# Optimization experiments

Measured on AMD Instinct MI355X. Metric: run time of the kernel, lower is better.

## Reference

```python
import jax, jax.numpy as jnp
import numpy as np

OBS, H, Z = 64, 128, 64
T, B = 512, 1024
EPS = 0.01


def _lin(x, W, b):
    # torch nn.Linear: y = x @ W.T + b, W: [out, in]
    return x @ W.T + b


def setup_inputs() -> dict:
    key = jax.random.key(0)
    ks = jax.random.split(key, 16)
    n = lambda k, shape: 0.1 * jax.random.normal(k, shape, dtype=jnp.float32)
    z = lambda shape: jnp.zeros(shape, dtype=jnp.float32)
    return {
        "s": jax.random.normal(ks[0], (T, B, OBS), dtype=jnp.float32),
        "noise": jax.random.normal(ks[1], (T, B, Z), dtype=jnp.float32),
        # phi_s / phi_z
        "W_phi_s": n(ks[2], (H, OBS)), "b_phi_s": z((H,)),
        "W_phi_z": n(ks[3], (H, Z)), "b_phi_z": z((H,)),
        # prior: Linear(H,H) ReLU Linear(H,2Z)
        "Wp1": n(ks[4], (H, H)), "bp1": z((H,)),
        "Wp2": n(ks[5], (2 * Z, H)), "bp2": z((2 * Z,)),
        # encoder: Linear(2H,H) ReLU Linear(H,2Z)
        "We1": n(ks[6], (H, 2 * H)), "be1": z((H,)),
        "We2": n(ks[7], (2 * Z, H)), "be2": z((2 * Z,)),
        # LSTMCell(input=2H, hidden=H), gate order i,f,g,o
        "W_ih": n(ks[8], (4 * H, 2 * H)), "b_ih": z((4 * H,)),
        "W_hh": n(ks[9], (4 * H, H)), "b_hh": z((4 * H,)),
        # decoder: Linear(2H,H) ReLU Linear(H,OBS)
        "Wd1": n(ks[10], (H, 2 * H)), "bd1": z((H,)),
        "Wd2": n(ks[11], (OBS, H)), "bd2": z((OBS,)),
    }


def reference(s, noise, W_phi_s, b_phi_s, W_phi_z, b_phi_z, Wp1, bp1, Wp2, bp2,
              We1, be1, We2, be2, W_ih, b_ih, W_hh, b_hh, Wd1, bd1, Wd2, bd2):
    h0 = jnp.zeros((s.shape[1], H), dtype=s.dtype)
    c0 = jnp.zeros((s.shape[1], H), dtype=s.dtype)

    def step(carry, xs):
        h, c, kl_acc, rc_acc = carry
        s_t, n_t = xs
        phi_s = _lin(s_t, W_phi_s, b_phi_s)                      # [B, H]
        # encoder on [phi_s, h]
        enc = _lin(jax.nn.relu(_lin(jnp.concatenate([phi_s, h], -1), We1, be1)), We2, be2)
        z_mu, z_std = jnp.split(enc, 2, axis=-1)
        z_std = jax.nn.softplus(z_std)
        # prior on h
        pri = _lin(jax.nn.relu(_lin(h, Wp1, bp1)), Wp2, bp2)
        p_mu, p_std = jnp.split(pri, 2, axis=-1)
        p_std = jax.nn.softplus(p_std)
        # reparameterize
        z_samp = z_mu + z_std * n_t
        phi_z = _lin(z_samp, W_phi_z, b_phi_z)                   # [B, H]
        # decode from [phi_z, h]
        recon = _lin(jax.nn.relu(_lin(jnp.concatenate([phi_z, h], -1), Wd1, bd1)), Wd2, bd2)
        # LSTM cell update with input [phi_s, phi_z]
        gates = _lin(jnp.concatenate([phi_s, phi_z], -1), W_ih, b_ih) + _lin(h, W_hh, b_hh)
        gi, gf, gg, go = jnp.split(gates, 4, axis=-1)
        c_new = jax.nn.sigmoid(gf) * c + jax.nn.sigmoid(gi) * jnp.tanh(gg)
        h_new = jax.nn.sigmoid(go) * jnp.tanh(c_new)
        # losses (sum over feature dim, mean over batch)
        rc_t = (0.5 * jnp.square(recon - s_t)).sum(-1).mean()
        kl_t = 0.5 * (2.0 * jnp.log(p_std + EPS) - 2.0 * jnp.log(z_std + EPS)
                      + (jnp.square(z_std) + jnp.square(z_mu - p_mu))
                      / (jnp.square(jnp.exp(p_std)) - 1.0)).sum(-1).mean()
        return (h_new, c_new, kl_acc + kl_t, rc_acc + rc_t), None

    (_, _, total_kl, total_rc), _ = jax.lax.scan(
        step, (h0, c0, jnp.float32(0.0), jnp.float32(0.0)), (s, noise))
    return total_kl + total_rc
```

## Files before the change

### kernel.cpp

```cpp
#include <hip/hip_runtime.h>

typedef __bf16 bf16_t;
typedef bf16_t bf16x8 __attribute__((ext_vector_type(8)));
typedef float  f32x4  __attribute__((ext_vector_type(4)));

#define TT 512
#define BB 1024

#define cL0   0
#define cL1   1024
#define cL2   3072
#define cL3   5120
#define cL4   7168
#define cL5   9216
#define cL6   10240
#define cL7   12288
#define cL8   13312
#define cL9   17408
#define cL10  21504
#define NCHUNK 29696

#define WS_FBIAS_OFF 475136
#define WS_FOLD_OFF  478208
#define WS_HSEQ_OFF  1048576
#define WS_NEED (WS_HSEQ_OFF + (size_t)TT * BB * 128 * 2)

__device__ __forceinline__ f32x4 mfma16(bf16x8 a, bf16x8 b, f32x4 c) {
  return __builtin_amdgcn_mfma_f32_16x16x32_bf16(a, b, c, 0, 0, 0);
}
__device__ __forceinline__ float sigm(float x) { return 1.0f / (1.0f + __expf(-x)); }
__device__ __forceinline__ float tanh_f(float x) {
  x = fminf(fmaxf(x, -15.0f), 15.0f);
  float e = __expf(2.0f * x);
  return (e - 1.0f) / (e + 1.0f);
}
__device__ __forceinline__ float softplus_f(float x) {
  return (x > 15.0f) ? x : __logf(1.0f + __expf(x));
}
__device__ __forceinline__ void wg_barrier() {
  asm volatile("s_waitcnt lgkmcnt(0)\n\ts_barrier" ::: "memory");
}
__device__ __forceinline__ void keep(bf16x8& v) { asm volatile("" : "+v"(v)); }

__global__ void vrnn_fold(const float* __restrict__ We1, const float* __restrict__ Wd1,
                          const float* __restrict__ Wih,
                          const float* __restrict__ Wps, const float* __restrict__ Wpz,
                          const float* __restrict__ bps, const float* __restrict__ bpz,
                          const float* __restrict__ be1, const float* __restrict__ bd1,
                          const float* __restrict__ bih, const float* __restrict__ bhh,
                          float* __restrict__ fold, float* __restrict__ fbias) {
  int id = blockIdx.x * 256 + threadIdx.x;
  if (id < 8192) {
    int n = id >> 6, k = id & 63; float acc = 0.f;
    for (int j = 0; j < 128; ++j) acc += We1[n*256 + j] * Wps[j*64 + k];
    fold[id] = acc;
  } else if (id < 16384) {
    int q = id - 8192; int n = q >> 6, k = q & 63; float acc = 0.f;
    for (int j = 0; j < 128; ++j) acc += Wd1[n*256 + j] * Wpz[j*64 + k];
    fold[id] = acc;
  } else if (id < 49152) {
    int q = id - 16384; int n = q >> 6, k = q & 63; float acc = 0.f;
    for (int j = 0; j < 128; ++j) acc += Wih[n*256 + j] * Wps[j*64 + k];
    fold[id] = acc;
  } else if (id < 81920) {
    int q = id - 49152; int n = q >> 6, k = q & 63; float acc = 0.f;
    for (int j = 0; j < 128; ++j) acc += Wih[n*256 + 128 + j] * Wpz[j*64 + k];
    fold[id] = acc;
  } else if (id < 82048) {
    int n = id - 81920; float acc = be1[n];
    for (int j = 0; j < 128; ++j) acc += We1[n*256 + j] * bps[j];
    fbias[n] = acc;
  } else if (id < 82176) {
    int n = id - 82048; float acc = bd1[n];
    for (int j = 0; j < 128; ++j) acc += Wd1[n*256 + j] * bpz[j];
    fbias[128 + n] = acc;
  } else if (id < 82688) {
    int n = id - 82176; float acc = bih[n] + bhh[n];
    for (int j = 0; j < 128; ++j) acc += Wih[n*256 + j]*bps[j] + Wih[n*256 + 128 + j]*bpz[j];
    fbias[256 + n] = acc;
  }
}

__global__ void vrnn_pack(const float* __restrict__ fold,
                          const float* __restrict__ We1, const float* __restrict__ We2,
                          const float* __restrict__ Wp1, const float* __restrict__ Wp2,
                          const float* __restrict__ Wd1, const float* __restrict__ Wd2,
                          const float* __restrict__ Whh,
                          bf16_t* __restrict__ packed) {
  int c = blockIdx.x * 256 + threadIdx.x;
  if (c >= NCHUNK) return;
  const float* src; int rs, co, Kt, base;
  if      (c < 1024)  { base = cL0;  src = fold;          rs = 64;  co = 0;   Kt = 2; }
  else if (c < 3072)  { base = cL1;  src = We1;           rs = 256; co = 128; Kt = 4; }
  else if (c < 5120)  { base = cL2;  src = We2;           rs = 128; co = 0;   Kt = 4; }
  else if (c < 7168)  { base = cL3;  src = Wp1;           rs = 128; co = 0;   Kt = 4; }
  else if (c < 9216)  { base = cL4;  src = Wp2;           rs = 128; co = 0;   Kt = 4; }
  else if (c < 10240) { base = cL5;  src = fold + 8192;   rs = 64;  co = 0;   Kt = 2; }
  else if (c < 12288) { base = cL6;  src = Wd1;           rs = 256; co = 128; Kt = 4; }
  else if (c < 13312) { base = cL7;  src = Wd2;           rs = 128; co = 0;   Kt = 4; }
  else if (c < 17408) { base = cL8;  src = fold + 16384;  rs = 64;  co = 0;   Kt = 2; }
  else if (c < 21504) { base = cL9;  src = fold + 49152;  rs = 64;  co = 0;   Kt = 2; }
  else                { base = cL10; src = Whh;           rs = 128; co = 0;   Kt = 4; }
  int local = c - base;
  int nt = local / (Kt * 64);
  int r = local - nt * Kt * 64;
  int kt = r >> 6, lane = r & 63;
  int n = nt * 16 + (lane & 15);
  int k = kt * 32 + (lane >> 4) * 8;
  const float* p = src + n * rs + co + k;
  bf16x8 v;
  #pragma unroll
  for (int j = 0; j < 8; ++j) v[j] = (bf16_t)p[j];
  *(bf16x8*)(packed + (size_t)c * 8) = v;
}

__global__ __launch_bounds__(512, 2) void vrnn_loop(
    const float* __restrict__ s, const float* __restrict__ noise,
    const bf16_t* __restrict__ packed, const float* __restrict__ fbias,
    const float* __restrict__ be2, bf16_t* __restrict__ hseq) {
  const bf16x8* Wf = (const bf16x8*)packed;

  __shared__ __align__(16) bf16_t A_h[2][16 * 136];
  __shared__ __align__(16) bf16_t A_s[2][16 * 72];
  __shared__ __align__(16) bf16_t A_z[16 * 72];
  __shared__ __align__(16) bf16_t A_e1[16 * 136];
  __shared__ float bsm[768];

  const int tid  = threadIdx.x;
  const int wv   = tid >> 6, ln = tid & 63;
  const int quad = ln >> 4, col = ln & 15;
  const int row0 = blockIdx.x * 16;
  const int pm_  = tid >> 5;
  const int pj   = (tid & 31) * 2;
  const int nloc0 = wv * 16 + col;
  const int j_own = wv * 16 + col;
  const int wq   = wv & 3;

  for (int i = tid; i < 768; i += 512) {
    float v;
    if      (i < 128) v = fbias[i];
    else if (i < 256) v = be2[i - 128];
    else              v = fbias[256 + (i - 256)];
    bsm[i] = v;
  }
  for (int i = tid; i < 16 * 136; i += 512) A_h[0][i] = (bf16_t)0.0f;
  {
    float2 v = *(const float2*)(s + ((size_t)0 * BB + row0 + pm_) * 64 + pj);
    A_s[0][pm_ * 72 + pj]     = (bf16_t)v.x;
    A_s[0][pm_ * 72 + pj + 1] = (bf16_t)v.y;
  }
  {
    unsigned long long* p = (unsigned long long*)(hseq + (size_t)row0 * 128);
    p[tid] = 0ull;
  }

  bf16x8 rb10[4][4];
  #pragma unroll
  for (int i = 0; i < 4; ++i) {
    int nt = wv + 8 * i;
    #pragma unroll
    for (int k = 0; k < 4; ++k) { rb10[i][k] = Wf[cL10 + (nt * 4 + k) * 64 + ln]; keep(rb10[i][k]); }
  }
  bf16x8 wE[6], rb8[4][2];
  wE[0] = Wf[cL0 + (wv * 2 + 0) * 64 + ln];
  wE[1] = Wf[cL0 + (wv * 2 + 1) * 64 + ln];
  #pragma unroll
  for (int k = 0; k < 4; ++k) wE[2 + k] = Wf[cL1 + (wv * 4 + k) * 64 + ln];
  #pragma unroll
  for (int i = 0; i < 4; ++i) {
    int nt = wv + 8 * i;
    rb8[i][0] = Wf[cL8 + (nt * 2 + 0) * 64 + ln];
    rb8[i][1] = Wf[cL8 + (nt * 2 + 1) * 64 + ln];
  }

  f32x4 c_reg = {0.f, 0.f, 0.f, 0.f};
  __syncthreads();

  int cb = 0;
  for (int t = 0; t < TT; ++t) {
    const int sb = t & 1;
    int zo = 0;
    asm volatile("" : "+s"(zo));
    const bf16x8* Wfv = Wf + zo;

    bf16x8 wmu[4], wsd[4];
    float nzr[4];
    if (wv < 4) {
      #pragma unroll
      for (int k = 0; k < 4; ++k) {
        wmu[k] = Wfv[cL2 + (wq * 4 + k) * 64 + ln];
        wsd[k] = Wfv[cL2 + ((wq + 4) * 4 + k) * 64 + ln];
      }
      #pragma unroll
      for (int r = 0; r < 4; ++r)
        nzr[r] = noise[((size_t)t * BB + row0 + quad * 4 + r) * 64 + j_own];
    }
    float2 svv = make_float2(0.f, 0.f);
    if (t + 1 < TT) svv = *(const float2*)(s + ((size_t)(t + 1) * BB + row0 + pm_) * 64 + pj);

    bf16x8 ah0 = *(const bf16x8*)&A_h[cb][col * 136 + 0 + quad * 8];
    bf16x8 ah1 = *(const bf16x8*)&A_h[cb][col * 136 + 32 + quad * 8];
    bf16x8 ah2 = *(const bf16x8*)&A_h[cb][col * 136 + 64 + quad * 8];
    bf16x8 ah3 = *(const bf16x8*)&A_h[cb][col * 136 + 96 + quad * 8];
    bf16x8 as0 = *(const bf16x8*)&A_s[sb][col * 72 + 0 + quad * 8];
    bf16x8 as1 = *(const bf16x8*)&A_s[sb][col * 72 + 32 + quad * 8];

    {
      float bv = bsm[nloc0];
      f32x4 c = {bv, bv, bv, bv};
      c = mfma16(as0, wE[0], c);
      c = mfma16(as1, wE[1], c);
      c = mfma16(ah0, wE[2], c);
      c = mfma16(ah1, wE[3], c);
      c = mfma16(ah2, wE[4], c);
      c = mfma16(ah3, wE[5], c);
      #pragma unroll
      for (int r = 0; r < 4; ++r)
        A_e1[(quad * 4 + r) * 136 + nloc0] = (bf16_t)fmaxf(c[r], 0.0f);
    }
    f32x4 Cg[4];
    #pragma unroll
    for (int i = 0; i < 4; ++i) {
      float bv = bsm[256 + j_own + 128 * i];
      f32x4 cc = {bv, bv, bv, bv};
      cc = mfma16(ah0, rb10[i][0], cc);
      cc = mfma16(ah1, rb10[i][1], cc);
      cc = mfma16(ah2, rb10[i][2], cc);
      cc = mfma16(ah3, rb10[i][3], cc);
      cc = mfma16(as0, rb8[i][0], cc);
      cc = mfma16(as1, rb8[i][1], cc);
      Cg[i] = cc;
    }
    wg_barrier();

    bf16x8 rb9[4][2];
    #pragma unroll
    for (int i = 0; i < 4; ++i) {
      int nt = wv + 8 * i;
      rb9[i][0] = Wfv[cL9 + (nt * 2 + 0) * 64 + ln];
      rb9[i][1] = Wfv[cL9 + (nt * 2 + 1) * 64 + ln];
    }
    if (wv < 4) {
      bf16x8 ae0 = *(const bf16x8*)&A_e1[col * 136 + 0 + quad * 8];
      bf16x8 ae1 = *(const bf16x8*)&A_e1[col * 136 + 32 + quad * 8];
      bf16x8 ae2 = *(const bf16x8*)&A_e1[col * 136 + 64 + quad * 8];
      bf16x8 ae3 = *(const bf16x8*)&A_e1[col * 136 + 96 + quad * 8];
      float bm = bsm[128 + wq * 16 + col], bs = bsm[128 + 64 + wq * 16 + col];
      f32x4 cm = {bm, bm, bm, bm};
      f32x4 cs = {bs, bs, bs, bs};
      cm = mfma16(ae0, wmu[0], cm); cs = mfma16(ae0, wsd[0], cs);
      cm = mfma16(ae1, wmu[1], cm); cs = mfma16(ae1, wsd[1], cs);
      cm = mfma16(ae2, wmu[2], cm); cs = mfma16(ae2, wsd[2], cs);
      cm = mfma16(ae3, wmu[3], cm); cs = mfma16(ae3, wsd[3], cs);
      #pragma unroll
      for (int r = 0; r < 4; ++r) {
        float z = cm[r] + softplus_f(cs[r]) * nzr[r];
        A_z[(quad * 4 + r) * 72 + wq * 16 + col] = (bf16_t)z;
      }
    }
    if (t + 1 < TT) {
      A_s[sb ^ 1][pm_ * 72 + pj]     = (bf16_t)svv.x;
      A_s[sb ^ 1][pm_ * 72 + pj + 1] = (bf16_t)svv.y;
    }
    wg_barrier();

    wE[0] = Wfv[cL0 + (wv * 2 + 0) * 64 + ln];
    wE[1] = Wfv[cL0 + (wv * 2 + 1) * 64 + ln];
    #pragma unroll
    for (int k = 0; k < 4; ++k) wE[2 + k] = Wfv[cL1 + (wv * 4 + k) * 64 + ln];
    #pragma unroll
    for (int i = 0; i < 4; ++i) {
      int nt = wv + 8 * i;
      rb8[i][0] = Wfv[cL8 + (nt * 2 + 0) * 64 + ln];
      rb8[i][1] = Wfv[cL8 + (nt * 2 + 1) * 64 + ln];
    }
    {
      bf16x8 az0 = *(const bf16x8*)&A_z[col * 72 + 0 + quad * 8];
      bf16x8 az1 = *(const bf16x8*)&A_z[col * 72 + 32 + quad * 8];
      #pragma unroll
      for (int i = 0; i < 4; ++i) {
        Cg[i] = mfma16(az0, rb9[i][0], Cg[i]);
        Cg[i] = mfma16(az1, rb9[i][1], Cg[i]);
      }
    }
    bf16_t* hp = hseq + (size_t)(t + 1) * BB * 128;
    #pragma unroll
    for (int r = 0; r < 4; ++r) {
      float gi = sigm(Cg[0][r]);
      float gf = sigm(Cg[1][r]);
      float gg = tanh_f(Cg[2][r]);
      float go = sigm(Cg[3][r]);
      float cn = gf * c_reg[r] + gi * gg;
      c_reg[r] = cn;
      bf16_t hv = (bf16_t)(go * tanh_f(cn));
      A_h[cb ^ 1][(quad * 4 + r) * 136 + j_own] = hv;
      if (t + 1 < TT) hp[(size_t)(row0 + quad * 4 + r) * 128 + j_own] = hv;
    }
    wg_barrier();
    cb ^= 1;
  }
}

__global__ __launch_bounds__(512, 2) void vrnn_tail(
    const float* __restrict__ s, const float* __restrict__ noise,
    const bf16_t* __restrict__ packed, const float* __restrict__ fbias,
    const float* __restrict__ bp1, const float* __restrict__ bp2,
    const float* __restrict__ be2, const float* __restrict__ bd2,
    const bf16_t* __restrict__ hseq, float* __restrict__ out) {
  const bf16x8* Wf = (const bf16x8*)packed;

  __shared__ __align__(16) bf16_t A_h[16 * 136];
  __shared__ __align__(16) bf16_t A_s[16 * 72];
  __shared__ __align__(16) bf16_t A_z[16 * 72];
  __shared__ __align__(16) bf16_t A_e1[16 * 136];
  __shared__ __align__(16) bf16_t A_p1[16 * 136];
  __shared__ __align__(16) bf16_t A_d1[16 * 136];
  __shared__ float zmu_s[16 * 68], zsd_s[16 * 68];
  __shared__ float dec2o[16 * 68];
  __shared__ float bsm[704];
  __shared__ float red[8];

  const int tid  = threadIdx.x;
  const int wv   = tid >> 6, ln = tid & 63;
  const int quad = ln >> 4, col = ln & 15;
  const int pm_  = tid >> 5;
  const int pj   = (tid & 31) * 2;
  const int nloc0 = wv * 16 + col;
  const int wq   = wv & 3;

  for (int i = tid; i < 704; i += 512) {
    float v;
    if      (i < 128) v = fbias[i];
    else if (i < 256) v = bp1[i - 128];
    else if (i < 384) v = be2[i - 256];
    else if (i < 512) v = bp2[i - 384];
    else if (i < 640) v = fbias[128 + (i - 512)];
    else              v = bd2[i - 640];
    bsm[i] = v;
  }

  bf16x8 wE[6], wP1[4], wmu[4], wsd[4], wD1[4], w5[2], w7[4];
  wE[0] = Wf[cL0 + (wv * 2 + 0) * 64 + ln];
  wE[1] = Wf[cL0 + (wv * 2 + 1) * 64 + ln];
  #pragma unroll
  for (int k = 0; k < 4; ++k) {
    wE[2 + k] = Wf[cL1 + (wv * 4 + k) * 64 + ln];
    wP1[k] = Wf[cL3 + (wv * 4 + k) * 64 + ln];
    wD1[k] = Wf[cL6 + (wv * 4 + k) * 64 + ln];
    w7[k]  = Wf[cL7 + (wq * 4 + k) * 64 + ln];
  }
  {
    int base2 = (wv < 4) ? cL2 : cL4;
    #pragma unroll
    for (int k = 0; k < 4; ++k) {
      wmu[k] = Wf[base2 + (wq * 4 + k) * 64 + ln];
      wsd[k] = Wf[base2 + ((wq + 4) * 4 + k) * 64 + ln];
    }
  }
  w5[0] = Wf[cL5 + (wv * 2 + 0) * 64 + ln];
  w5[1] = Wf[cL5 + (wv * 2 + 1) * 64 + ln];
  #pragma unroll
  for (int k = 0; k < 6; ++k) keep(wE[k]);
  #pragma unroll
  for (int k = 0; k < 4; ++k) { keep(wP1[k]); keep(wmu[k]); keep(wsd[k]); keep(wD1[k]); keep(w7[k]); }
  keep(w5[0]); keep(w5[1]);

  float kl_acc = 0.0f, rc_acc = 0.0f;
  __syncthreads();

  const int hm  = tid >> 5;
  const int hc4 = (tid & 31) * 4;

  for (int tau = blockIdx.x; tau < TT * 64; tau += gridDim.x) {
    const int t = tau >> 6;
    const int row0 = (tau & 63) * 16;

    {
      unsigned long long hv = *(const unsigned long long*)(
          hseq + (size_t)t * BB * 128 + (size_t)(row0 + hm) * 128 + hc4);
      *(unsigned long long*)&A_h[hm * 136 + hc4] = hv;
    }
    float2 sv = *(const float2*)(s + ((size_t)t * BB + row0 + pm_) * 64 + pj);
    A_s[pm_ * 72 + pj]     = (bf16_t)sv.x;
    A_s[pm_ * 72 + pj + 1] = (bf16_t)sv.y;
    float nzr[4];
    if (wv < 4) {
      #pragma unroll
      for (int r = 0; r < 4; ++r)
        nzr[r] = noise[((size_t)t * BB + row0 + quad * 4 + r) * 64 + wq * 16 + col];
    }
    wg_barrier();

    bf16x8 ah0 = *(const bf16x8*)&A_h[col * 136 + 0 + quad * 8];
    bf16x8 ah1 = *(const bf16x8*)&A_h[col * 136 + 32 + quad * 8];
    bf16x8 ah2 = *(const bf16x8*)&A_h[col * 136 + 64 + quad * 8];
    bf16x8 ah3 = *(const bf16x8*)&A_h[col * 136 + 96 + quad * 8];
    bf16x8 as0 = *(const bf16x8*)&A_s[col * 72 + 0 + quad * 8];
    bf16x8 as1 = *(const bf16x8*)&A_s[col * 72 + 32 + quad * 8];
    {
      float bv = bsm[nloc0];
      f32x4 c = {bv, bv, bv, bv};
      c = mfma16(as0, wE[0], c);
      c = mfma16(as1, wE[1], c);
      c = mfma16(ah0, wE[2], c);
      c = mfma16(ah1, wE[3], c);
      c = mfma16(ah2, wE[4], c);
      c = mfma16(ah3, wE[5], c);
      #pragma unroll
      for (int r = 0; r < 4; ++r)
        A_e1[(quad * 4 + r) * 136 + nloc0] = (bf16_t)fmaxf(c[r], 0.0f);
    }
    {
      float bv = bsm[128 + nloc0];
      f32x4 c = {bv, bv, bv, bv};
      c = mfma16(ah0, wP1[0], c);
      c = mfma16(ah1, wP1[1], c);
      c = mfma16(ah2, wP1[2], c);
      c = mfma16(ah3, wP1[3], c);
      #pragma unroll
      for (int r = 0; r < 4; ++r)
        A_p1[(quad * 4 + r) * 136 + nloc0] = (bf16_t)fmaxf(c[r], 0.0f);
    }
    wg_barrier();

    float Pmu[4], Pps[4];
    if (wv < 4) {
      bf16x8 ae0 = *(const bf16x8*)&A_e1[col * 136 + 0 + quad * 8];
      bf16x8 ae1 = *(const bf16x8*)&A_e1[col * 136 + 32 + quad * 8];
      bf16x8 ae2 = *(const bf16x8*)&A_e1[col * 136 + 64 + quad * 8];
      bf16x8 ae3 = *(const bf16x8*)&A_e1[col * 136 + 96 + quad * 8];
      float bm = bsm[256 + wq * 16 + col], bs = bsm[256 + 64 + wq * 16 + col];
      f32x4 cm = {bm, bm, bm, bm};
      f32x4 cs = {bs, bs, bs, bs};
      cm = mfma16(ae0, wmu[0], cm); cs = mfma16(ae0, wsd[0], cs);
      cm = mfma16(ae1, wmu[1], cm); cs = mfma16(ae1, wsd[1], cs);
      cm = mfma16(ae2, wmu[2], cm); cs = mfma16(ae2, wsd[2], cs);
      cm = mfma16(ae3, wmu[3], cm); cs = mfma16(ae3, wsd[3], cs);
      #pragma unroll
      for (int r = 0; r < 4; ++r) {
        float zm = cm[r];
        float zs = softplus_f(cs[r]);
        int m = quad * 4 + r;
        A_z[m * 72 + wq * 16 + col] = (bf16_t)(zm + zs * nzr[r]);
        zmu_s[m * 68 + wq * 16 + col] = zm;
        zsd_s[m * 68 + wq * 16 + col] = zs;
      }
    } else {
      bf16x8 ap0 = *(const bf16x8*)&A_p1[col * 136 + 0 + quad * 8];
      bf16x8 ap1 = *(const bf16x8*)&A_p1[col * 136 + 32 + quad * 8];
      bf16x8 ap2 = *(const bf16x8*)&A_p1[col * 136 + 64 + quad * 8];
      bf16x8 ap3 = *(const bf16x8*)&A_p1[col * 136 + 96 + quad * 8];
      float bm = bsm[384 + wq * 16 + col], bs = bsm[384 + 64 + wq * 16 + col];
      f32x4 cm = {bm, bm, bm, bm};
      f32x4 cs = {bs, bs, bs, bs};
      cm = mfma16(ap0, wmu[0], cm); cs = mfma16(ap0, wsd[0], cs);
      cm = mfma16(ap1, wmu[1], cm); cs = mfma16(ap1, wsd[1], cs);
      cm = mfma16(ap2, wmu[2], cm); cs = mfma16(ap2, wsd[2], cs);
      cm = mfma16(ap3, wmu[3], cm); cs = mfma16(ap3, wsd[3], cs);
      #pragma unroll
      for (int r = 0; r < 4; ++r) { Pmu[r] = cm[r]; Pps[r] = softplus_f(cs[r]); }
    }
    wg_barrier();

    {
      bf16x8 az0 = *(const bf16x8*)&A_z[col * 72 + 0 + quad * 8];
      bf16x8 az1 = *(const bf16x8*)&A_z[col * 72 + 32 + quad * 8];
      float bv = bsm[512 + nloc0];
      f32x4 c = {bv, bv, bv, bv};
      c = mfma16(az0, w5[0], c);
      c = mfma16(az1, w5[1], c);
      c = mfma16(ah0, wD1[0], c);
      c = mfma16(ah1, wD1[1], c);
      c = mfma16(ah2, wD1[2], c);
      c = mfma16(ah3, wD1[3], c);
      #pragma unroll
      for (int r = 0; r < 4; ++r)
        A_d1[(quad * 4 + r) * 136 + nloc0] = (bf16_t)fmaxf(c[r], 0.0f);
    }
    if (wv >= 4) {
      #pragma unroll
      for (int r = 0; r < 4; ++r) {
        int m = quad * 4 + r;
        float zm = zmu_s[m * 68 + wq * 16 + col];
        float zs = zsd_s[m * 68 + wq * 16 + col];
        float dm = zm - Pmu[r];
        float ps = Pps[r];
        float den = __expf(2.0f * ps) - 1.0f;
        kl_acc += 0.5f * (2.0f * __logf(ps + 0.01f) - 2.0f * __logf(zs + 0.01f)
                          + (zs * zs + dm * dm) / den);
      }
    }
    wg_barrier();

    if (wv >= 4) {
      bf16x8 ad0 = *(const bf16x8*)&A_d1[col * 136 + 0 + quad * 8];
      bf16x8 ad1 = *(const bf16x8*)&A_d1[col * 136 + 32 + quad * 8];
      bf16x8 ad2 = *(const bf16x8*)&A_d1[col * 136 + 64 + quad * 8];
      bf16x8 ad3 = *(const bf16x8*)&A_d1[col * 136 + 96 + quad * 8];
      float bv = bsm[640 + wq * 16 + col];
      f32x4 c = {bv, bv, bv, bv};
      c = mfma16(ad0, w7[0], c);
      c = mfma16(ad1, w7[1], c);
      c = mfma16(ad2, w7[2], c);
      c = mfma16(ad3, w7[3], c);
      #pragma unroll
      for (int r = 0; r < 4; ++r)
        dec2o[(quad * 4 + r) * 68 + wq * 16 + col] = c[r];
    }
    wg_barrier();
    {
      float d0 = dec2o[pm_ * 68 + pj] - sv.x;
      float d1 = dec2o[pm_ * 68 + pj + 1] - sv.y;
      rc_acc += 0.5f * (d0 * d0 + d1 * d1);
    }
  }

  float tot = (kl_acc + rc_acc) * (1.0f / 1024.0f);
  #pragma unroll
  for (int off = 32; off > 0; off >>= 1) tot += __shfl_down(tot, off);
  if (ln == 0) red[wv] = tot;
  __syncthreads();
  if (tid == 0) {
    float sum = 0.f;
    #pragma unroll
    for (int i = 0; i < 8; ++i) sum += red[i];
    atomicAdd(out, sum);
  }
}

__global__ __launch_bounds__(512, 2) void vrnn_mono(
    const float* __restrict__ s, const float* __restrict__ noise,
    const bf16_t* __restrict__ packed, const float* __restrict__ fbias,
    const float* __restrict__ bp1, const float* __restrict__ bp2,
    const float* __restrict__ be2, const float* __restrict__ bd2,
    float* __restrict__ out) {
  const bf16x8* Wf = (const bf16x8*)packed;
  __shared__ __align__(16) bf16_t A_h[16 * 136];
  __shared__ __align__(16) bf16_t A_s[2][16 * 72];
  __shared__ __align__(16) bf16_t A_z[16 * 72];
  __shared__ __align__(16) bf16_t A_e1[16 * 136];
  __shared__ __align__(16) bf16_t A_p1[16 * 136];
  __shared__ __align__(16) bf16_t A_d1[16 * 136];
  __shared__ float zmu_s[16 * 68], zsd_s[16 * 68];
  __shared__ float dec2o[16 * 68];
  __shared__ float bsm[1216];
  __shared__ float red[8];
  const int tid  = threadIdx.x;
  const int wv   = tid >> 6, ln = tid & 63;
  const int quad = ln >> 4, col = ln & 15;
  const int row0 = blockIdx.x * 16;
  const int pm_  = tid >> 5;
  const int pj   = (tid & 31) * 2;
  const int nloc0 = wv * 16 + col;
  const int j_own = wv * 16 + col;
  const int wq   = wv & 3;
  for (int i = tid; i < 1216; i += 512) {
    float v;
    if      (i < 128)  v = fbias[i];
    else if (i < 256)  v = bp1[i - 128];
    else if (i < 384)  v = be2[i - 256];
    else if (i < 512)  v = bp2[i - 384];
    else if (i < 640)  v = fbias[128 + (i - 512)];
    else if (i < 704)  v = bd2[i - 640];
    else               v = fbias[256 + (i - 704)];
    bsm[i] = v;
  }
  for (int i = tid; i < 16 * 136; i += 512) A_h[i] = (bf16_t)0.0f;
  {
    float2 v = *(const float2*)(s + ((size_t)0 * BB + row0 + pm_) * 64 + pj);
    A_s[0][pm_ * 72 + pj]     = (bf16_t)v.x;
    A_s[0][pm_ * 72 + pj + 1] = (bf16_t)v.y;
  }
  bf16x8 rb9[4][2], rb10[4][4];
  #pragma unroll
  for (int i = 0; i < 4; ++i) {
    int nt = wv + 8 * i;
    rb9[i][0] = Wf[cL9 + (nt * 2 + 0) * 64 + ln];
    rb9[i][1] = Wf[cL9 + (nt * 2 + 1) * 64 + ln];
    #pragma unroll
    for (int k = 0; k < 4; ++k) rb10[i][k] = Wf[cL10 + (nt * 4 + k) * 64 + ln];
  }
  bf16x8 wE0[2], wE1[4];
  wE0[0] = Wf[cL0 + (wv * 2 + 0) * 64 + ln];
  wE0[1] = Wf[cL0 + (wv * 2 + 1) * 64 + ln];
  #pragma unroll
  for (int k = 0; k < 4; ++k) wE1[k] = Wf[cL1 + (wv * 4 + k) * 64 + ln];
  bf16x8 wmu[4], wsd[4];
  {
    int base2 = (wv < 4) ? cL2 : cL4;
    #pragma unroll
    for (int k = 0; k < 4; ++k) {
      wmu[k] = Wf[base2 + (wq * 4 + k) * 64 + ln];
      wsd[k] = Wf[base2 + ((wq + 4) * 4 + k) * 64 + ln];
    }
  }
  f32x4 c_reg = {0.f, 0.f, 0.f, 0.f};
  float kl_acc = 0.0f, rc_acc = 0.0f;
  __syncthreads();
  for (int t = 0; t < TT; ++t) {
    const int sb = t & 1;
    float nzr[4];
    if (wv < 4) {
      #pragma unroll
      for (int r = 0; r < 4; ++r)
        nzr[r] = noise[((size_t)t * BB + row0 + quad * 4 + r) * 64 + j_own];
    }
    float2 svv = make_float2(0.f, 0.f);
    if (t + 1 < TT) svv = *(const float2*)(s + ((size_t)(t + 1) * BB + row0 + pm_) * 64 + pj);
    float2 spv = make_float2(0.f, 0.f);
    if (t > 0) spv = *(const float2*)(s + ((size_t)(t - 1) * BB + row0 + pm_) * 64 + pj);
    bf16x8 w8[4][2], wP1[4], wD1[4];
    #pragma unroll
    for (int i = 0; i < 4; ++i) {
      int nt = wv + 8 * i;
      w8[i][0] = Wf[cL8 + (nt * 2 + 0) * 64 + ln];
      w8[i][1] = Wf[cL8 + (nt * 2 + 1) * 64 + ln];
    }
    #pragma unroll
    for (int k = 0; k < 4; ++k) {
      wP1[k] = Wf[cL3 + (wv * 4 + k) * 64 + ln];
      wD1[k] = Wf[cL6 + (wv * 4 + k) * 64 + ln];
    }
    bf16x8 ah0 = *(const bf16x8*)&A_h[col * 136 + 0 + quad * 8];
    bf16x8 ah1 = *(const bf16x8*)&A_h[col * 136 + 32 + quad * 8];
    bf16x8 ah2 = *(const bf16x8*)&A_h[col * 136 + 64 + quad * 8];
    bf16x8 ah3 = *(const bf16x8*)&A_h[col * 136 + 96 + quad * 8];
    bf16x8 as0 = *(const bf16x8*)&A_s[sb][col * 72 + 0 + quad * 8];
    bf16x8 as1 = *(const bf16x8*)&A_s[sb][col * 72 + 32 + quad * 8];
    {
      float bv = bsm[nloc0];
      f32x4 c = {bv, bv, bv, bv};
      c = mfma16(as0, wE0[0], c);
      c = mfma16(as1, wE0[1], c);
      c = mfma16(ah0, wE1[0], c);
      c = mfma16(ah1, wE1[1], c);
      c = mfma16(ah2, wE1[2], c);
      c = mfma16(ah3, wE1[3], c);
      #pragma unroll
      for (int r = 0; r < 4; ++r)
        A_e1[(quad * 4 + r) * 136 + nloc0] = (bf16_t)fmaxf(c[r], 0.0f);
    }
    f32x4 Cg[4];
    #pragma unroll
    for (int i = 0; i < 4; ++i) {
      float bv = bsm[704 + j_own + 128 * i];
      f32x4 cc = {bv, bv, bv, bv};
      cc = mfma16(ah0, rb10[i][0], cc);
      cc = mfma16(ah1, rb10[i][1], cc);
      cc = mfma16(ah2, rb10[i][2], cc);
      cc = mfma16(ah3, rb10[i][3], cc);
      cc = mfma16(as0, w8[i][0], cc);
      cc = mfma16(as1, w8[i][1], cc);
      Cg[i] = cc;
    }
    {
      float bv = bsm[128 + nloc0];
      f32x4 c = {bv, bv, bv, bv};
      c = mfma16(ah0, wP1[0], c);
      c = mfma16(ah1, wP1[1], c);
      c = mfma16(ah2, wP1[2], c);
      c = mfma16(ah3, wP1[3], c);
      #pragma unroll
      for (int r = 0; r < 4; ++r)
        A_p1[(quad * 4 + r) * 136 + nloc0] = (bf16_t)fmaxf(c[r], 0.0f);
    }
    f32x4 Cd;
    {
      float bv = bsm[512 + nloc0];
      f32x4 c = {bv, bv, bv, bv};
      c = mfma16(ah0, wD1[0], c);
      c = mfma16(ah1, wD1[1], c);
      c = mfma16(ah2, wD1[2], c);
      c = mfma16(ah3, wD1[3], c);
      Cd = c;
    }
    if (wv >= 4 && t > 0) {
      bf16x8 ad0 = *(const bf16x8*)&A_d1[col * 136 + 0 + quad * 8];
      bf16x8 ad1 = *(const bf16x8*)&A_d1[col * 136 + 32 + quad * 8];
      bf16x8 ad2 = *(const bf16x8*)&A_d1[col * 136 + 64 + quad * 8];
      bf16x8 ad3 = *(const bf16x8*)&A_d1[col * 136 + 96 + quad * 8];
      bf16x8 w7[4];
      #pragma unroll
      for (int k = 0; k < 4; ++k) w7[k] = Wf[cL7 + (wq * 4 + k) * 64 + ln];
      float bv = bsm[640 + wq * 16 + col];
      f32x4 c = {bv, bv, bv, bv};
      c = mfma16(ad0, w7[0], c);
      c = mfma16(ad1, w7[1], c);
      c = mfma16(ad2, w7[2], c);
      c = mfma16(ad3, w7[3], c);
      #pragma unroll
      for (int r = 0; r < 4; ++r)
        dec2o[(quad * 4 + r) * 68 + wq * 16 + col] = c[r];
    }
    wg_barrier();
    float Pmu[4], Pps[4];
    if (wv < 4) {
      bf16x8 ae0 = *(const bf16x8*)&A_e1[col * 136 + 0 + quad * 8];
      bf16x8 ae1 = *(const bf16x8*)&A_e1[col * 136 + 32 + quad * 8];
      bf16x8 ae2 = *(const bf16x8*)&A_e1[col * 136 + 64 + quad * 8];
      bf16x8 ae3 = *(const bf16x8*)&A_e1[col * 136 + 96 + quad * 8];
      float bm = bsm[256 + wq * 16 + col], bs = bsm[256 + 64 + wq * 16 + col];
      f32x4 cm = {bm, bm, bm, bm};
      f32x4 cs = {bs, bs, bs, bs};
      cm = mfma16(ae0, wmu[0], cm); cs = mfma16(ae0, wsd[0], cs);
      cm = mfma16(ae1, wmu[1], cm); cs = mfma16(ae1, wsd[1], cs);
      cm = mfma16(ae2, wmu[2], cm); cs = mfma16(ae2, wsd[2], cs);
      cm = mfma16(ae3, wmu[3], cm); cs = mfma16(ae3, wsd[3], cs);
      #pragma unroll
      for (int r = 0; r < 4; ++r) {
        float zm = cm[r];
        float zs = softplus_f(cs[r]);
        float z = zm + zs * nzr[r];
        int m = quad * 4 + r;
        A_z[m * 72 + j_own] = (bf16_t)z;
        zmu_s[m * 68 + j_own] = zm;
        zsd_s[m * 68 + j_own] = zs;
      }
    } else {
      bf16x8 ap0 = *(const bf16x8*)&A_p1[col * 136 + 0 + quad * 8];
      bf16x8 ap1 = *(const bf16x8*)&A_p1[col * 136 + 32 + quad * 8];
      bf16x8 ap2 = *(const bf16x8*)&A_p1[col * 136 + 64 + quad * 8];
      bf16x8 ap3 = *(const bf16x8*)&A_p1[col * 136 + 96 + quad * 8];
      float bm = bsm[384 + wq * 16 + col], bs = bsm[384 + 64 + wq * 16 + col];
      f32x4 cm = {bm, bm, bm, bm};
      f32x4 cs = {bs, bs, bs, bs};
      cm = mfma16(ap0, wmu[0], cm); cs = mfma16(ap0, wsd[0], cs);
      cm = mfma16(ap1, wmu[1], cm); cs = mfma16(ap1, wsd[1], cs);
      cm = mfma16(ap2, wmu[2], cm); cs = mfma16(ap2, wsd[2], cs);
      cm = mfma16(ap3, wmu[3], cm); cs = mfma16(ap3, wsd[3], cs);
      #pragma unroll
      for (int r = 0; r < 4; ++r) { Pmu[r] = cm[r]; Pps[r] = softplus_f(cs[r]); }
    }
    if (t > 0) {
      float d0 = dec2o[pm_ * 68 + pj] - spv.x;
      float d1 = dec2o[pm_ * 68 + pj + 1] - spv.y;
      rc_acc += 0.5f * (d0 * d0 + d1 * d1);
    }
    if (t + 1 < TT) {
      A_s[sb ^ 1][pm_ * 72 + pj]     = (bf16_t)svv.x;
      A_s[sb ^ 1][pm_ * 72 + pj + 1] = (bf16_t)svv.y;
    }
    wg_barrier();
    bf16x8 az0 = *(const bf16x8*)&A_z[col * 72 + 0 + quad * 8];
    bf16x8 az1 = *(const bf16x8*)&A_z[col * 72 + 32 + quad * 8];
    #pragma unroll
    for (int i = 0; i < 4; ++i) {
      Cg[i] = mfma16(az0, rb9[i][0], Cg[i]);
      Cg[i] = mfma16(az1, rb9[i][1], Cg[i]);
    }
    {
      bf16x8 w5a = Wf[cL5 + (wv * 2 + 0) * 64 + ln];
      bf16x8 w5b = Wf[cL5 + (wv * 2 + 1) * 64 + ln];
      Cd = mfma16(az0, w5a, Cd);
      Cd = mfma16(az1, w5b, Cd);
      #pragma unroll
      for (int r = 0; r < 4; ++r)
        A_d1[(quad * 4 + r) * 136 + nloc0] = (bf16_t)fmaxf(Cd[r], 0.0f);
    }
    #pragma unroll
    for (int r = 0; r < 4; ++r) {
      float gi = sigm(Cg[0][r]);
      float gf = sigm(Cg[1][r]);
      float gg = tanh_f(Cg[2][r]);
      float go = sigm(Cg[3][r]);
      float cn = gf * c_reg[r] + gi * gg;
      c_reg[r] = cn;
      A_h[(quad * 4 + r) * 136 + j_own] = (bf16_t)(go * tanh_f(cn));
    }
    if (wv >= 4) {
      #pragma unroll
      for (int r = 0; r < 4; ++r) {
        int m = quad * 4 + r;
        float zm = zmu_s[m * 68 + wq * 16 + col];
        float zs = zsd_s[m * 68 + wq * 16 + col];
        float dm = zm - Pmu[r];
        float ps = Pps[r];
        float den = __expf(2.0f * ps) - 1.0f;
        kl_acc += 0.5f * (2.0f * __logf(ps + 0.01f) - 2.0f * __logf(zs + 0.01f)
                          + (zs * zs + dm * dm) / den);
      }
    }
    wg_barrier();
  }
  if (wv >= 4) {
    bf16x8 ad0 = *(const bf16x8*)&A_d1[col * 136 + 0 + quad * 8];
    bf16x8 ad1 = *(const bf16x8*)&A_d1[col * 136 + 32 + quad * 8];
    bf16x8 ad2 = *(const bf16x8*)&A_d1[col * 136 + 64 + quad * 8];
    bf16x8 ad3 = *(const bf16x8*)&A_d1[col * 136 + 96 + quad * 8];
    bf16x8 w7[4];
    #pragma unroll
    for (int k = 0; k < 4; ++k) w7[k] = Wf[cL7 + (wq * 4 + k) * 64 + ln];
    float bv = bsm[640 + wq * 16 + col];
    f32x4 c = {bv, bv, bv, bv};
    c = mfma16(ad0, w7[0], c);
    c = mfma16(ad1, w7[1], c);
    c = mfma16(ad2, w7[2], c);
    c = mfma16(ad3, w7[3], c);
    #pragma unroll
    for (int r = 0; r < 4; ++r)
      dec2o[(quad * 4 + r) * 68 + wq * 16 + col] = c[r];
  }
  __syncthreads();
  {
    float2 sl = *(const float2*)(s + ((size_t)(TT - 1) * BB + row0 + pm_) * 64 + pj);
    float d0 = dec2o[pm_ * 68 + pj] - sl.x;
    float d1 = dec2o[pm_ * 68 + pj + 1] - sl.y;
    rc_acc += 0.5f * (d0 * d0 + d1 * d1);
  }
  float tot = (kl_acc + rc_acc) * (1.0f / 1024.0f);
  #pragma unroll
  for (int off = 32; off > 0; off >>= 1) tot += __shfl_down(tot, off);
  if (ln == 0) red[wv] = tot;
  __syncthreads();
  if (tid == 0) {
    float sum = 0.f;
    #pragma unroll
    for (int i = 0; i < 8; ++i) sum += red[i];
    atomicAdd(out, sum);
  }
}

extern "C" void kernel_launch(void* const* d_in, const int* in_sizes, int n_in,
                              void* d_out, int out_size, void* d_ws, size_t ws_size,
                              hipStream_t stream) {
  (void)in_sizes; (void)n_in; (void)out_size;
  const float* s   = (const float*)d_in[0];
  const float* nz  = (const float*)d_in[1];
  const float* Wps = (const float*)d_in[2];
  const float* bps = (const float*)d_in[3];
  const float* Wpz = (const float*)d_in[4];
  const float* bpz = (const float*)d_in[5];
  const float* Wp1 = (const float*)d_in[6];
  const float* bp1 = (const float*)d_in[7];
  const float* Wp2 = (const float*)d_in[8];
  const float* bp2 = (const float*)d_in[9];
  const float* We1 = (const float*)d_in[10];
  const float* be1 = (const float*)d_in[11];
  const float* We2 = (const float*)d_in[12];
  const float* be2 = (const float*)d_in[13];
  const float* Wih = (const float*)d_in[14];
  const float* bih = (const float*)d_in[15];
  const float* Whh = (const float*)d_in[16];
  const float* bhh = (const float*)d_in[17];
  const float* Wd1 = (const float*)d_in[18];
  const float* bd1 = (const float*)d_in[19];
  const float* Wd2 = (const float*)d_in[20];
  const float* bd2 = (const float*)d_in[21];

  bf16_t* packed = (bf16_t*)d_ws;
  float* fbias = (float*)((char*)d_ws + WS_FBIAS_OFF);
  float* fold  = (float*)((char*)d_ws + WS_FOLD_OFF);
  bf16_t* hseq = (bf16_t*)((char*)d_ws + WS_HSEQ_OFF);

  hipMemsetAsync(d_out, 0, sizeof(float), stream);
  vrnn_fold<<<(82688 + 255) / 256, 256, 0, stream>>>(We1, Wd1, Wih, Wps, Wpz, bps, bpz,
                                                     be1, bd1, bih, bhh, fold, fbias);
  vrnn_pack<<<(NCHUNK + 255) / 256, 256, 0, stream>>>(fold, We1, We2, Wp1, Wp2, Wd1, Wd2,
                                                      Whh, packed);
  if (ws_size >= WS_NEED) {
    vrnn_loop<<<64, 512, 0, stream>>>(s, nz, packed, fbias, be2, hseq);
    vrnn_tail<<<256, 512, 0, stream>>>(s, nz, packed, fbias, bp1, bp2, be2, bd2, hseq,
                                       (float*)d_out);
  } else {
    vrnn_mono<<<64, 512, 0, stream>>>(s, nz, packed, fbias, bp1, bp2, be2, bd2,
                                      (float*)d_out);
  }
}
```

Before: 2.188 ms.

## Keep LSTM/encoder weights in registers, stage encoder-2 weights in LDS, prefetch noise/s

Loads the rb8, rb9 and wE weight fragments into registers once before the time loop instead of reloading them from global memory every step. The encoder second-layer weights (mu/std) are copied into a new 32 KB LDS buffer and read from there each step. Noise and next-step s values are prefetched one step ahead to hide global latency. This raises register and LDS pressure, which may hurt occupancy at launch bounds (512,2) or cause spills.

```diff
diff --git a/kernel.cpp b/kernel.cpp
--- a/kernel.cpp
+++ b/kernel.cpp
@@ -124,6 +124,7 @@
   __shared__ __align__(16) bf16_t A_s[2][16 * 72];
   __shared__ __align__(16) bf16_t A_z[16 * 72];
   __shared__ __align__(16) bf16_t A_e1[16 * 136];
+  __shared__ __align__(16) bf16_t Wmu_lds[2048 * 8];
   __shared__ float bsm[768];
 
   const int tid  = threadIdx.x;
@@ -143,6 +144,10 @@
     else              v = fbias[256 + (i - 256)];
     bsm[i] = v;
   }
+  {
+    bf16x8* wl = (bf16x8*)Wmu_lds;
+    for (int c = tid; c < 2048; c += 512) wl[c] = Wf[cL2 + c];
+  }
   for (int i = tid; i < 16 * 136; i += 512) A_h[0][i] = (bf16_t)0.0f;
   {
     float2 v = *(const float2*)(s + ((size_t)0 * BB + row0 + pm_) * 64 + pj);
@@ -154,24 +159,29 @@
     p[tid] = 0ull;
   }
 
-  bf16x8 rb10[4][4];
+  bf16x8 rb10[4][4], rb8[4][2], rb9[4][2], wE[6];
   #pragma unroll
   for (int i = 0; i < 4; ++i) {
     int nt = wv + 8 * i;
     #pragma unroll
     for (int k = 0; k < 4; ++k) { rb10[i][k] = Wf[cL10 + (nt * 4 + k) * 64 + ln]; keep(rb10[i][k]); }
-  }
-  bf16x8 wE[6], rb8[4][2];
-  wE[0] = Wf[cL0 + (wv * 2 + 0) * 64 + ln];
-  wE[1] = Wf[cL0 + (wv * 2 + 1) * 64 + ln];
-  #pragma unroll
-  for (int k = 0; k < 4; ++k) wE[2 + k] = Wf[cL1 + (wv * 4 + k) * 64 + ln];
-  #pragma unroll
-  for (int i = 0; i < 4; ++i) {
-    int nt = wv + 8 * i;
-    rb8[i][0] = Wf[cL8 + (nt * 2 + 0) * 64 + ln];
-    rb8[i][1] = Wf[cL8 + (nt * 2 + 1) * 64 + ln];
-  }
+    rb8[i][0] = Wf[cL8 + (nt * 2 + 0) * 64 + ln]; keep(rb8[i][0]);
+    rb8[i][1] = Wf[cL8 + (nt * 2 + 1) * 64 + ln]; keep(rb8[i][1]);
+    rb9[i][0] = Wf[cL9 + (nt * 2 + 0) * 64 + ln]; keep(rb9[i][0]);
+    rb9[i][1] = Wf[cL9 + (nt * 2 + 1) * 64 + ln]; keep(rb9[i][1]);
+  }
+  wE[0] = Wf[cL0 + (wv * 2 + 0) * 64 + ln]; keep(wE[0]);
+  wE[1] = Wf[cL0 + (wv * 2 + 1) * 64 + ln]; keep(wE[1]);
+  #pragma unroll
+  for (int k = 0; k < 4; ++k) { wE[2 + k] = Wf[cL1 + (wv * 4 + k) * 64 + ln]; keep(wE[2 + k]); }
+
+  float nzr[4] = {0.f, 0.f, 0.f, 0.f};
+  if (wv < 4) {
+    #pragma unroll
+    for (int r = 0; r < 4; ++r)
+      nzr[r] = noise[((size_t)0 * BB + row0 + quad * 4 + r) * 64 + j_own];
+  }
+  float2 svN = *(const float2*)(s + ((size_t)1 * BB + row0 + pm_) * 64 + pj);
 
   f32x4 c_reg = {0.f, 0.f, 0.f, 0.f};
   __syncthreads();
@@ -179,24 +189,6 @@
   int cb = 0;
   for (int t = 0; t < TT; ++t) {
     const int sb = t & 1;
-    int zo = 0;
-    asm volatile("" : "+s"(zo));
-    const bf16x8* Wfv = Wf + zo;
-
-    bf16x8 wmu[4], wsd[4];
-    float nzr[4];
-    if (wv < 4) {
-      #pragma unroll
-      for (int k = 0; k < 4; ++k) {
-        wmu[k] = Wfv[cL2 + (wq * 4 + k) * 64 + ln];
-        wsd[k] = Wfv[cL2 + ((wq + 4) * 4 + k) * 64 + ln];
-      }
-      #pragma unroll
-      for (int r = 0; r < 4; ++r)
-        nzr[r] = noise[((size_t)t * BB + row0 + quad * 4 + r) * 64 + j_own];
-    }
-    float2 svv = make_float2(0.f, 0.f);
-    if (t + 1 < TT) svv = *(const float2*)(s + ((size_t)(t + 1) * BB + row0 + pm_) * 64 + pj);
 
     bf16x8 ah0 = *(const bf16x8*)&A_h[cb][col * 136 + 0 + quad * 8];
     bf16x8 ah1 = *(const bf16x8*)&A_h[cb][col * 136 + 32 + quad * 8];
@@ -233,47 +225,49 @@
     }
     wg_barrier();
 
-    bf16x8 rb9[4][2];
-    #pragma unroll
-    for (int i = 0; i < 4; ++i) {
-      int nt = wv + 8 * i;
-      rb9[i][0] = Wfv[cL9 + (nt * 2 + 0) * 64 + ln];
-      rb9[i][1] = Wfv[cL9 + (nt * 2 + 1) * 64 + ln];
-    }
-    if (wv < 4) {
-      bf16x8 ae0 = *(const bf16x8*)&A_e1[col * 136 + 0 + quad * 8];
-      bf16x8 ae1 = *(const bf16x8*)&A_e1[col * 136 + 32 + quad * 8];
-      bf16x8 ae2 = *(const bf16x8*)&A_e1[col * 136 + 64 + quad * 8];
-      bf16x8 ae3 = *(const bf16x8*)&A_e1[col * 136 + 96 + quad * 8];
-      float bm = bsm[128 + wq * 16 + col], bs = bsm[128 + 64 + wq * 16 + col];
-      f32x4 cm = {bm, bm, bm, bm};
-      f32x4 cs = {bs, bs, bs, bs};
-      cm = mfma16(ae0, wmu[0], cm); cs = mfma16(ae0, wsd[0], cs);
-      cm = mfma16(ae1, wmu[1], cm); cs = mfma16(ae1, wsd[1], cs);
-      cm = mfma16(ae2, wmu[2], cm); cs = mfma16(ae2, wsd[2], cs);
-      cm = mfma16(ae3, wmu[3], cm); cs = mfma16(ae3, wsd[3], cs);
-      #pragma unroll
-      for (int r = 0; r < 4; ++r) {
-        float z = cm[r] + softplus_f(cs[r]) * nzr[r];
-        A_z[(quad * 4 + r) * 72 + wq * 16 + col] = (bf16_t)z;
+    {
+      int lzo = 0;
+      asm volatile("" : "+s"(lzo));
+      const bf16x8* Wml = (const bf16x8*)Wmu_lds + lzo;
+      if (wv < 4) {
+        bf16x8 wmu[4], wsd[4];
+        #pragma unroll
+        for (int k = 0; k < 4; ++k) {
+          wmu[k] = Wml[(wq * 4 + k) * 64 + ln];
+          wsd[k] = Wml[((wq + 4) * 4 + k) * 64 + ln];
+        }
+        bf16x8 ae0 = *(const bf16x8*)&A_e1[col * 136 + 0 + quad * 8];
+        bf16x8 ae1 = *(const bf16x8*)&A_e1[col * 136 + 32 + quad * 8];
+        bf16x8 ae2 = *(const bf16x8*)&A_e1[col * 136 + 64 + quad * 8];
+        bf16x8 ae3 = *(const bf16x8*)&A_e1[col * 136 + 96 + quad * 8];
+        float bm = bsm[128 + wq * 16 + col], bs = bsm[128 + 64 + wq * 16 + col];
+        f32x4 cm = {bm, bm, bm, bm};
+        f32x4 cs = {bs, bs, bs, bs};
+        cm = mfma16(ae0, wmu[0], cm); cs = mfma16(ae0, wsd[0], cs);
+        cm = mfma16(ae1, wmu[1], cm); cs = mfma16(ae1, wsd[1], cs);
+        cm = mfma16(ae2, wmu[2], cm); cs = mfma16(ae2, wsd[2], cs);
+        cm = mfma16(ae3, wmu[3], cm); cs = mfma16(ae3, wsd[3], cs);
+        #pragma unroll
+        for (int r = 0; r < 4; ++r) {
+          float z = cm[r] + softplus_f(cs[r]) * nzr[r];
+          A_z[(quad * 4 + r) * 72 + wq * 16 + col] = (bf16_t)z;
+        }
       }
     }
     if (t + 1 < TT) {
-      A_s[sb ^ 1][pm_ * 72 + pj]     = (bf16_t)svv.x;
-      A_s[sb ^ 1][pm_ * 72 + pj + 1] = (bf16_t)svv.y;
-    }
-    wg_barrier();
-
-    wE[0] = Wfv[cL0 + (wv * 2 + 0) * 64 + ln];
-    wE[1] = Wfv[cL0 + (wv * 2 + 1) * 64 + ln];
-    #pragma unroll
-    for (int k = 0; k < 4; ++k) wE[2 + k] = Wfv[cL1 + (wv * 4 + k) * 64 + ln];
-    #pragma unroll
-    for (int i = 0; i < 4; ++i) {
-      int nt = wv + 8 * i;
-      rb8[i][0] = Wfv[cL8 + (nt * 2 + 0) * 64 + ln];
-      rb8[i][1] = Wfv[cL8 + (nt * 2 + 1) * 64 + ln];
-    }
+      A_s[sb ^ 1][pm_ * 72 + pj]     = (bf16_t)svN.x;
+      A_s[sb ^ 1][pm_ * 72 + pj + 1] = (bf16_t)svN.y;
+    }
+    wg_barrier();
+
+    if (wv < 4 && t + 1 < TT) {
+      #pragma unroll
+      for (int r = 0; r < 4; ++r)
+        nzr[r] = noise[((size_t)(t + 1) * BB + row0 + quad * 4 + r) * 64 + j_own];
+    }
+    if (t + 2 < TT)
+      svN = *(const float2*)(s + ((size_t)(t + 2) * BB + row0 + pm_) * 64 + pj);
+
     {
       bf16x8 az0 = *(const bf16x8*)&A_z[col * 72 + 0 + quad * 8];
       bf16x8 az1 = *(const bf16x8*)&A_z[col * 72 + 32 + quad * 8];
```

Result: faster. 1.868 ms (-14.6%).
